# Kernel optimization log

Hardware: AMD Instinct MI355X
Metric: run time of the kernel (lower is better)

The kernel has to match this reference:

```python
import jax, jax.numpy as jnp
import numpy as np


def _binarize_except_outliers(weight):
    # torch.mean / torch.std over the flattened weight; torch.std is unbiased (ddof=1)
    mean = jnp.mean(weight)
    std = jnp.std(weight, ddof=1)
    lower = mean - std
    upper = mean + std
    outliers = (weight < lower) | (weight > upper)
    # non-outliers -> sign(w) (STEBinary forward); outliers keep original fp values
    return jnp.where(outliers, weight, jnp.sign(weight))


def setup_inputs() -> dict:
    key = jax.random.key(0)
    k1, k2, k3 = jax.random.split(key, 3)
    B, S, D_IN, D_OUT = 8, 2048, 4096, 4096
    x = jax.random.normal(k1, (B, S, D_IN), dtype=jnp.float32)
    weight = jax.random.normal(k2, (D_OUT, D_IN), dtype=jnp.float32) * 0.02
    bias = jax.random.normal(k3, (D_OUT,), dtype=jnp.float32) * 0.02
    return {"x": x, "weight": weight, "bias": bias}


def reference(x, weight, bias):
    w_bin = _binarize_except_outliers(weight)  # [d_out, d_in]
    # F.linear: x @ w.T + b
    out = jnp.einsum("bsd,od->bso", x, w_bin) + bias
    return out
```

## Files before the change

### kernel.cpp

```cpp
#include <hip/hip_runtime.h>
#include <stdint.h>
#include <math.h>

typedef __attribute__((ext_vector_type(8))) short short8;
typedef __attribute__((ext_vector_type(4))) float f32x4;

typedef const __attribute__((address_space(1))) void* gas_ptr;
typedef __attribute__((address_space(3))) void* las_ptr;

__device__ __forceinline__ void gld_lds16(const void* g, void* l) {
    __builtin_amdgcn_global_load_lds((gas_ptr)g, (las_ptr)l, 16, 0, 0);
}

__device__ __forceinline__ unsigned short f32_to_bf16_rne(float f) {
    unsigned u = __builtin_bit_cast(unsigned, f);
    u += 0x7FFFu + ((u >> 16) & 1u);
    return (unsigned short)(u >> 16);
}

__global__ void stats_partial_kernel(const float* __restrict__ w, int n4, double* __restrict__ partials) {
    __shared__ double ssum[256];
    __shared__ double ssq[256];
    int t = threadIdx.x;
    long i = (long)blockIdx.x * blockDim.x + t;
    long stride = (long)gridDim.x * blockDim.x;
    double s = 0.0, q = 0.0;
    for (; i < n4; i += stride) {
        float4 v = ((const float4*)w)[i];
        s += (double)v.x + (double)v.y + (double)v.z + (double)v.w;
        q += (double)v.x * v.x + (double)v.y * v.y + (double)v.z * v.z + (double)v.w * v.w;
    }
    ssum[t] = s; ssq[t] = q;
    __syncthreads();
    for (int off = 128; off > 0; off >>= 1) {
        if (t < off) { ssum[t] += ssum[t + off]; ssq[t] += ssq[t + off]; }
        __syncthreads();
    }
    if (t == 0) {
        partials[2 * blockIdx.x]     = ssum[0];
        partials[2 * blockIdx.x + 1] = ssq[0];
    }
}

__global__ void stats_final_kernel(const double* __restrict__ partials, int nblocks, long n,
                                   float* __restrict__ bounds) {
    __shared__ double ssum[256];
    __shared__ double ssq[256];
    int t = threadIdx.x;
    double s = 0.0, q = 0.0;
    for (int i = t; i < nblocks; i += 256) {
        s += partials[2 * i];
        q += partials[2 * i + 1];
    }
    ssum[t] = s; ssq[t] = q;
    __syncthreads();
    for (int off = 128; off > 0; off >>= 1) {
        if (t < off) { ssum[t] += ssum[t + off]; ssq[t] += ssq[t + off]; }
        __syncthreads();
    }
    if (t == 0) {
        double sum = ssum[0], sumsq = ssq[0];
        double mean = sum / (double)n;
        double var = (sumsq - sum * sum / (double)n) / (double)(n - 1);
        double sd = sqrt(var);
        bounds[0] = (float)(mean - sd);
        bounds[1] = (float)(mean + sd);
    }
}

__global__ void binarize_w_kernel(const float* __restrict__ w, const float* __restrict__ bounds,
                                  unsigned short* __restrict__ wb, long n8) {
    float lo = bounds[0], hi = bounds[1];
    long i = (long)blockIdx.x * blockDim.x + threadIdx.x;
    long stride = (long)gridDim.x * blockDim.x;
    for (; i < n8; i += stride) {
        float4 v0 = ((const float4*)w)[2 * i];
        float4 v1 = ((const float4*)w)[2 * i + 1];
        float r[8] = {v0.x, v0.y, v0.z, v0.w, v1.x, v1.y, v1.z, v1.w};
        short8 o;
#pragma unroll
        for (int j = 0; j < 8; j++) {
            float f = r[j];
            bool outlier = (f < lo) || (f > hi);
            float b = outlier ? f : (f > 0.f ? 1.f : (f < 0.f ? -1.f : 0.f));
            o[j] = (short)f32_to_bf16_rne(b);
        }
        ((short8*)wb)[i] = o;
    }
}

__global__ void convert_x_kernel(const float* __restrict__ x, unsigned short* __restrict__ xb, long n8) {
    long i = (long)blockIdx.x * blockDim.x + threadIdx.x;
    long stride = (long)gridDim.x * blockDim.x;
    for (; i < n8; i += stride) {
        float4 v0 = ((const float4*)x)[2 * i];
        float4 v1 = ((const float4*)x)[2 * i + 1];
        short8 o;
        o[0] = (short)f32_to_bf16_rne(v0.x);
        o[1] = (short)f32_to_bf16_rne(v0.y);
        o[2] = (short)f32_to_bf16_rne(v0.z);
        o[3] = (short)f32_to_bf16_rne(v0.w);
        o[4] = (short)f32_to_bf16_rne(v1.x);
        o[5] = (short)f32_to_bf16_rne(v1.y);
        o[6] = (short)f32_to_bf16_rne(v1.z);
        o[7] = (short)f32_to_bf16_rne(v1.w);
        ((short8*)xb)[i] = o;
    }
}

#define BM 256
#define BN 256
#define BK 64

__global__ __launch_bounds__(512, 2) void gemm_8phase_kernel(
    const unsigned short* __restrict__ A,
    const unsigned short* __restrict__ B,
    const float* __restrict__ bias,
    float* __restrict__ C,
    int M, int N, int K)
{
    __shared__ __align__(16) unsigned short As[2][BM * BK];
    __shared__ __align__(16) unsigned short Bs[2][BN * BK];

    const int t = threadIdx.x;
    const int wave = t >> 6;
    const int lane = t & 63;
    const int wm = wave >> 2;
    const int wn = wave & 3;
    const int lm = lane & 15;
    const int quad = lane >> 4;

    const int nwg = gridDim.x;
    int id = blockIdx.x;
    if ((nwg & 7) == 0) id = (id & 7) * (nwg >> 3) + (id >> 3);
    const int nbn = N / BN;
    const int tile_m = (id / nbn) * BM;
    const int tile_n = (id % nbn) * BN;

    const int srow = t >> 3;
    const int scol = ((t & 7) ^ (srow & 7)) * 8;
    const int lds_wbase = wave * 512;

    const unsigned short* Abase = A + (size_t)tile_m * K;
    const unsigned short* Bbase = B + (size_t)tile_n * K;

    auto stageA = [&](int u2, int h) {
        const unsigned short* g = Abase + (size_t)(h * 128 + srow) * K + u2 * BK + scol;
        unsigned short* l = &As[u2 & 1][h * 8192 + lds_wbase];
        gld_lds16(g, l);
        gld_lds16(g + (size_t)64 * K, l + 4096);
    };
    auto stageB = [&](int u2, int h) {
        const unsigned short* g = Bbase + (size_t)(h * 128 + srow) * K + u2 * BK + scol;
        unsigned short* l = &Bs[u2 & 1][h * 8192 + lds_wbase];
        gld_lds16(g, l);
        gld_lds16(g + (size_t)64 * K, l + 4096);
    };

    stageB(0, 0); stageB(0, 1); stageA(0, 0); stageA(0, 1);
    stageB(1, 0); stageB(1, 1); stageA(1, 0);
    asm volatile("s_waitcnt vmcnt(6)" ::: "memory");
    __builtin_amdgcn_s_barrier();

    f32x4 acc[8][4] = {};
    short8 bf[4][2];

    const int NT = K / BK;
    for (int u = 0; u < NT; ++u) {
        const unsigned short* as = &As[u & 1][0];
        const unsigned short* bs = &Bs[u & 1][0];
        const bool s1 = (u + 1 < NT);
        const bool s2 = (u + 2 < NT);

#pragma unroll
        for (int q = 0; q < 4; ++q) {
            if (q == 0)      { if (s1) stageA(u + 1, 1); }
            else if (q == 1) { if (s2) stageB(u + 2, 0); }
            else if (q == 2) { if (s2) stageB(u + 2, 1); }
            else             { if (s2) stageA(u + 2, 0); }

            if (q == 0) {
#pragma unroll
                for (int j = 0; j < 4; ++j) {
                    int brow = wn * 64 + j * 16 + lm;
#pragma unroll
                    for (int ks = 0; ks < 2; ++ks)
                        bf[j][ks] = *(const short8*)&bs[brow * 64 + (((ks * 4 + quad) ^ (brow & 7)) * 8)];
                }
            }
            short8 af[2][2];
            const int arow0 = q * 64 + wm * 32 + lm;
#pragma unroll
            for (int i = 0; i < 2; ++i) {
                int arow = arow0 + i * 16;
#pragma unroll
                for (int ks = 0; ks < 2; ++ks)
                    af[i][ks] = *(const short8*)&as[arow * 64 + (((ks * 4 + quad) ^ (arow & 7)) * 8)];
            }

            __builtin_amdgcn_s_barrier();
            asm volatile("s_waitcnt lgkmcnt(0)" ::: "memory");
            __builtin_amdgcn_s_setprio(1);
#pragma unroll
            for (int ks = 0; ks < 2; ++ks)
#pragma unroll
                for (int i = 0; i < 2; ++i)
#pragma unroll
                    for (int j = 0; j < 4; ++j)
                        acc[q * 2 + i][j] = __builtin_amdgcn_mfma_f32_16x16x32_bf16(
                            af[i][ks], bf[j][ks], acc[q * 2 + i][j], 0, 0, 0);
            __builtin_amdgcn_s_setprio(0);

            if (q == 3) {
                if (s2)      { asm volatile("s_waitcnt vmcnt(6)" ::: "memory"); }
                else if (s1) { asm volatile("s_waitcnt vmcnt(0)" ::: "memory"); }
            }
            __builtin_amdgcn_s_barrier();
        }
    }

#pragma unroll
    for (int j = 0; j < 4; ++j) {
        const int col = tile_n + wn * 64 + j * 16 + lm;
        const float bv = bias[col];
#pragma unroll
        for (int m = 0; m < 8; ++m) {
            const int row0 = tile_m + (m >> 1) * 64 + wm * 32 + (m & 1) * 16 + quad * 4;
#pragma unroll
            for (int r = 0; r < 4; ++r)
                C[(size_t)(row0 + r) * N + col] = acc[m][j][r] + bv;
        }
    }
}

__global__ void gemm_fallback_kernel(const float* __restrict__ A, const float* __restrict__ W,
                                     const float* __restrict__ bias, const float* __restrict__ bounds,
                                     float* __restrict__ C, int M, int N, int K) {
    __shared__ float as[16][16];
    __shared__ float wsm[16][17];
    int tx = threadIdx.x, ty = threadIdx.y;
    int row = blockIdx.y * 16 + ty;
    int col = blockIdx.x * 16 + tx;
    float lo = bounds[0], hi = bounds[1];
    float acc = 0.f;
    for (int k0 = 0; k0 < K; k0 += 16) {
        as[ty][tx] = A[(size_t)row * K + k0 + tx];
        float wv = W[(size_t)(blockIdx.x * 16 + ty) * K + k0 + tx];
        bool outlier = (wv < lo) || (wv > hi);
        wsm[ty][tx] = outlier ? wv : (wv > 0.f ? 1.f : (wv < 0.f ? -1.f : 0.f));
        __syncthreads();
#pragma unroll
        for (int k = 0; k < 16; k++) acc += as[ty][k] * wsm[tx][k];
        __syncthreads();
    }
    C[(size_t)row * N + col] = acc + bias[col];
}

extern "C" void kernel_launch(void* const* d_in, const int* in_sizes, int n_in,
                              void* d_out, int out_size, void* d_ws, size_t ws_size,
                              hipStream_t stream) {
    const float* x    = (const float*)d_in[0];
    const float* w    = (const float*)d_in[1];
    const float* bias = (const float*)d_in[2];
    float* out = (float*)d_out;

    const int  N  = in_sizes[2];
    const long wn = (long)in_sizes[1];
    const int  K  = (int)(wn / N);
    const long xn = (long)in_sizes[0];
    const int  M  = (int)(xn / K);

    char* ws = (char*)d_ws;
    float*  bounds   = (float*)ws;
    double* partials = (double*)(ws + 64);
    const size_t wb_off = 16512;
    unsigned short* wb = (unsigned short*)(ws + wb_off);
    const size_t xb_off = wb_off + (size_t)wn * 2;
    unsigned short* xb = (unsigned short*)(ws + xb_off);
    const size_t need_full = xb_off + (size_t)xn * 2;

    stats_partial_kernel<<<1024, 256, 0, stream>>>(w, (int)(wn / 4), partials);
    stats_final_kernel<<<1, 256, 0, stream>>>(partials, 1024, wn, bounds);

    const bool ok256 = (M % 256 == 0) && (N % 256 == 0) && (K % 64 == 0) && (K / 64 >= 3)
                       && (wn % 8 == 0) && (xn % 8 == 0);

    if (ws_size >= need_full && ok256) {
        long wn8 = wn / 8, xn8 = xn / 8;
        int bb = (int)((wn8 + 255) / 256); if (bb > 2048) bb = 2048;
        int cb = (int)((xn8 + 255) / 256); if (cb > 2048) cb = 2048;
        binarize_w_kernel<<<bb, 256, 0, stream>>>(w, bounds, wb, wn8);
        convert_x_kernel<<<cb, 256, 0, stream>>>(x, xb, xn8);
        dim3 grid((M / BM) * (N / BN));
        gemm_8phase_kernel<<<grid, 512, 0, stream>>>(xb, wb, bias, out, M, N, K);
    } else {
        dim3 grid(N / 16, M / 16), blk(16, 16);
        gemm_fallback_kernel<<<grid, blk, 0, stream>>>(x, w, bias, bounds, out, M, N, K);
    }
}
```

Before: 1.083 ms.

## Software-pipeline LDS A-fragment reads one quarter ahead of MFMAs

Restructures the per-K-tile inner loop so the A fragments for the next quarter-tile are read from shared memory while the MFMAs for the current quarter run. This replaces the barrier plus explicit lgkmcnt(0) wait before each MFMA group, halving the barriers per K-tile from eight to four. The aim is to hide LDS read latency and cut synchronisation stalls. In exchange, more fragment registers stay live at once, which may raise VGPR pressure. It also relies on the barrier placement still keeping the async global-to-LDS stages away from data that is still being read.

```diff
diff --git a/kernel.cpp b/kernel.cpp
--- a/kernel.cpp
+++ b/kernel.cpp
@@ -163,7 +163,6 @@
     __builtin_amdgcn_s_barrier();
 
     f32x4 acc[8][4] = {};
-    short8 bf[4][2];
 
     const int NT = K / BK;
     for (int u = 0; u < NT; ++u) {
@@ -172,34 +171,18 @@
         const bool s1 = (u + 1 < NT);
         const bool s2 = (u + 2 < NT);
 
-#pragma unroll
-        for (int q = 0; q < 4; ++q) {
-            if (q == 0)      { if (s1) stageA(u + 1, 1); }
-            else if (q == 1) { if (s2) stageB(u + 2, 0); }
-            else if (q == 2) { if (s2) stageB(u + 2, 1); }
-            else             { if (s2) stageA(u + 2, 0); }
-
-            if (q == 0) {
-#pragma unroll
-                for (int j = 0; j < 4; ++j) {
-                    int brow = wn * 64 + j * 16 + lm;
-#pragma unroll
-                    for (int ks = 0; ks < 2; ++ks)
-                        bf[j][ks] = *(const short8*)&bs[brow * 64 + (((ks * 4 + quad) ^ (brow & 7)) * 8)];
-                }
-            }
-            short8 af[2][2];
-            const int arow0 = q * 64 + wm * 32 + lm;
+        short8 bf[4][2];
+
+        auto lda = [&](short8 (&af)[2][2], int q) {
 #pragma unroll
             for (int i = 0; i < 2; ++i) {
-                int arow = arow0 + i * 16;
+                int arow = q * 64 + wm * 32 + i * 16 + lm;
 #pragma unroll
                 for (int ks = 0; ks < 2; ++ks)
                     af[i][ks] = *(const short8*)&as[arow * 64 + (((ks * 4 + quad) ^ (arow & 7)) * 8)];
             }
-
-            __builtin_amdgcn_s_barrier();
-            asm volatile("s_waitcnt lgkmcnt(0)" ::: "memory");
+        };
+        auto mm = [&](short8 (&af)[2][2], int q) {
             __builtin_amdgcn_s_setprio(1);
 #pragma unroll
             for (int ks = 0; ks < 2; ++ks)
@@ -210,13 +193,39 @@
                         acc[q * 2 + i][j] = __builtin_amdgcn_mfma_f32_16x16x32_bf16(
                             af[i][ks], bf[j][ks], acc[q * 2 + i][j], 0, 0, 0);
             __builtin_amdgcn_s_setprio(0);
-
-            if (q == 3) {
-                if (s2)      { asm volatile("s_waitcnt vmcnt(6)" ::: "memory"); }
-                else if (s1) { asm volatile("s_waitcnt vmcnt(0)" ::: "memory"); }
-            }
-            __builtin_amdgcn_s_barrier();
+        };
+
+        if (s1) stageA(u + 1, 1);
+#pragma unroll
+        for (int j = 0; j < 4; ++j) {
+            int brow = wn * 64 + j * 16 + lm;
+#pragma unroll
+            for (int ks = 0; ks < 2; ++ks)
+                bf[j][ks] = *(const short8*)&bs[brow * 64 + (((ks * 4 + quad) ^ (brow & 7)) * 8)];
         }
+        short8 af0[2][2], af1[2][2];
+        lda(af0, 0);
+        lda(af1, 1);
+        mm(af0, 0);
+        __builtin_amdgcn_s_barrier();
+
+        if (s2) stageB(u + 2, 0);
+        short8 af2[2][2];
+        lda(af2, 2);
+        mm(af1, 1);
+        __builtin_amdgcn_s_barrier();
+
+        if (s2) stageB(u + 2, 1);
+        short8 af3[2][2];
+        lda(af3, 3);
+        mm(af2, 2);
+        __builtin_amdgcn_s_barrier();
+
+        if (s2) stageA(u + 2, 0);
+        mm(af3, 3);
+        if (s2)      { asm volatile("s_waitcnt vmcnt(6)" ::: "memory"); }
+        else if (s1) { asm volatile("s_waitcnt vmcnt(0)" ::: "memory"); }
+        __builtin_amdgcn_s_barrier();
     }
 
 #pragma unroll
```

Result: faster. 1.049 ms (-3.1%).
